# Performance work log

Hardware: AMD Instinct MI355X
Metric: run time of the kernel (lower is better)

The kernel has to match this reference:

```python
import jax, jax.numpy as jnp
import numpy as np

K = 5            # top-k prototypes
EMBED = 256      # per-pixel embedding dim
HIDDEN = 512     # MLP hidden dim
N_LIB = 16384    # lab index size
N_BANDS = 224    # spectral bands of prototype spectra


def setup_inputs() -> dict:
    key = jax.random.key(0)
    ks = jax.random.split(key, 12)
    b, h, w = 2, 128, 128
    inp = {
        "features": jax.random.normal(ks[0], (b, h, w, EMBED), dtype=jnp.float32),
        # score_proj MLP: embed -> hidden -> k
        "w1_s": jax.random.normal(ks[1], (EMBED, HIDDEN), dtype=jnp.float32) / np.sqrt(EMBED),
        "b1_s": jnp.zeros((HIDDEN,), dtype=jnp.float32),
        "w2_s": jax.random.normal(ks[2], (HIDDEN, K), dtype=jnp.float32) / np.sqrt(HIDDEN),
        "b2_s": jnp.zeros((K,), dtype=jnp.float32),
        # abundance_proj MLP: embed+k -> hidden -> k+2
        "w1_a": jax.random.normal(ks[3], (EMBED + K, HIDDEN), dtype=jnp.float32) / np.sqrt(EMBED + K),
        "b1_a": jnp.zeros((HIDDEN,), dtype=jnp.float32),
        "w2_a": jax.random.normal(ks[4], (HIDDEN, K + 2), dtype=jnp.float32) / np.sqrt(HIDDEN),
        "b2_a": jnp.zeros((K + 2,), dtype=jnp.float32),
        # LabIndex library embeddings (cosine-similarity index) and prototype spectra
        "lab_library": jax.random.normal(ks[5], (N_LIB, EMBED), dtype=jnp.float32),
        "prototype_spectra": jax.random.normal(ks[6], (N_LIB, N_BANDS), dtype=jnp.float32),
    }
    return inp


def _mlp(x, w1, b1, w2, b2):
    return jnp.maximum(x @ w1 + b1, 0.0) @ w2 + b2


def reference(features, w1_s, b1_s, w2_s, b2_s, w1_a, b1_a, w2_a, b2_a,
              lab_library, prototype_spectra):
    b, h, w, c = features.shape
    flat = features.reshape(-1, c)                      # [P, C]

    scores = _mlp(flat, w1_s, b1_s, w2_s, b2_s)         # [P, K]

    # batched kNN query (replaces per-pixel Python loop); cosine similarity top-k
    eps = 1e-12
    fn = flat / (jnp.linalg.norm(flat, axis=-1, keepdims=True) + eps)
    ln = lab_library / (jnp.linalg.norm(lab_library, axis=-1, keepdims=True) + eps)
    sims = fn @ ln.T                                    # [P, N_LIB]
    cand_sims, cand_ids = jax.lax.top_k(sims, K)        # [P, K] each

    fused = jnp.concatenate([flat, scores], axis=-1)    # [P, C+K]
    abundance_logits = _mlp(fused, w1_a, b1_a, w2_a, b2_a)  # [P, K+2]
    abundances = jax.nn.softmax(abundance_logits, axis=-1)

    protos = prototype_spectra[cand_ids]                # [P, K, N_BANDS]
    recon = jnp.sum(abundances[:, :K, None] * protos, axis=1)  # [P, N_BANDS]

    best = jnp.argmax(abundances[:, :K], axis=-1)       # [P]
    dominant = jnp.take_along_axis(cand_ids, best[:, None], axis=1)[:, 0]

    return (dominant.reshape(b, h, w),
            abundances.reshape(b, h, w, -1),
            recon.reshape(b, h, w, -1),
            cand_sims.reshape(b, h, w, -1))
```

## Files before the change

kernel.cpp:

```cpp
#include <hip/hip_runtime.h>
#include <math.h>

#define EMB 256
#define HID 512
#define KTOP 5
#define NLIB 16384
#define NB 224
#define P_TOT 32768

#define OUT_DOM ((size_t)0)
#define OUT_AB  ((size_t)P_TOT)
#define OUT_RE  ((size_t)8 * P_TOT)
#define OUT_CS  ((size_t)232 * P_TOT)

#define WS_SCORES 0
#define WS_INVL   (P_TOT * KTOP * 4)
#define WS_IDS8   (WS_INVL + NLIB * 4)
#define WS_CIDS   (WS_IDS8 + P_TOT * 8 * 4)
#define WS_LAB    (WS_CIDS + P_TOT * 5 * 4)

typedef __attribute__((ext_vector_type(8))) short short8;
typedef __attribute__((ext_vector_type(4))) float f32x4;
typedef __attribute__((ext_vector_type(16))) float f32x16;

__device__ __forceinline__ unsigned short f2bf(float x) {
  unsigned int u = __float_as_uint(x);
  u += 0x7fffu + ((u >> 16) & 1u);
  return (unsigned short)(u >> 16);
}
__device__ __forceinline__ float bf2f(unsigned short b) {
  return __uint_as_float(((unsigned int)b) << 16);
}

__device__ __forceinline__ bool better_(float v, int vi, float e, int ei) {
  return (v > e) || ((v == e) && (vi < ei));
}
__device__ __forceinline__ bool betterd_(double v, int vi, double e, int ei) {
  return (v > e) || ((v == e) && (vi < ei));
}

__device__ __forceinline__ void ins5_(float& s0, int& d0, float& s1, int& d1,
                                      float& s2, int& d2, float& s3, int& d3,
                                      float& s4, int& d4, float v, int vi) {
  if (!better_(v, vi, s4, d4)) return;
  s4 = v; d4 = vi;
  if (better_(s4, d4, s3, d3)) {
    float tf = s3; int td = d3; s3 = s4; d3 = d4; s4 = tf; d4 = td;
    if (better_(s3, d3, s2, d2)) {
      tf = s2; td = d2; s2 = s3; d2 = d3; s3 = tf; d3 = td;
      if (better_(s2, d2, s1, d1)) {
        tf = s1; td = d1; s1 = s2; d1 = d2; s2 = tf; d2 = td;
        if (better_(s1, d1, s0, d0)) {
          tf = s0; td = d0; s0 = s1; d0 = d1; s1 = tf; d1 = td;
        }
      }
    }
  }
}

__device__ __forceinline__ void ins8_(float m[8], int n[8], float v, int vi) {
  if (!better_(v, vi, m[7], n[7])) return;
  m[7] = v; n[7] = vi;
  #pragma unroll
  for (int q = 7; q >= 1; --q) {
    if (better_(m[q], n[q], m[q - 1], n[q - 1])) {
      float tf = m[q - 1]; m[q - 1] = m[q]; m[q] = tf;
      int td = n[q - 1]; n[q - 1] = n[q]; n[q] = td;
    }
  }
}

__global__ __launch_bounds__(64) void labsplit_kernel(const float* __restrict__ lab,
                                                      char* __restrict__ wslab) {
  const int row = blockIdx.x;
  const int lane = threadIdx.x;
  const int k16 = lane >> 2, sub = lane & 3;
  float4 v = *(const float4*)(lab + (size_t)row * EMB + k16 * 16 + sub * 4);
  ushort4 ph, pl;
  ph.x = f2bf(v.x); pl.x = f2bf(v.x - bf2f(ph.x));
  ph.y = f2bf(v.y); pl.y = f2bf(v.y - bf2f(ph.y));
  ph.z = f2bf(v.z); pl.z = f2bf(v.z - bf2f(ph.z));
  ph.w = f2bf(v.w); pl.w = f2bf(v.w - bf2f(ph.w));
  const size_t cbase = (size_t)((row >> 8) * 16 + k16) * 16384;
  const size_t off = cbase + (size_t)(row & 255) * 32 + sub * 8;
  *(ushort4*)(wslab + off) = ph;
  *(ushort4*)(wslab + off + 8192) = pl;
}

__global__ __launch_bounds__(64) void libnorm_kernel(const float* __restrict__ lab,
                                                     float* __restrict__ invl) {
  const int row = blockIdx.x;
  const int lane = threadIdx.x;
  float4 v = *(const float4*)(lab + (size_t)row * EMB + lane * 4);
  float s = v.x * v.x + v.y * v.y + v.z * v.z + v.w * v.w;
  #pragma unroll
  for (int off = 32; off >= 1; off >>= 1) s += __shfl_down(s, off);
  if (lane == 0) invl[row] = 1.0f / (sqrtf(s) + 1e-12f);
}

__global__ __launch_bounds__(256) void score_mlp_kernel(
    const float* __restrict__ feat, const float* __restrict__ w1,
    const float* __restrict__ b1, const float* __restrict__ w2,
    const float* __restrict__ b2, float* __restrict__ scores) {
  __shared__ __align__(16) float xs[16 * 264];
  __shared__ __align__(16) float hs[16 * 516];
  const int t = threadIdx.x;
  const int pb = blockIdx.x * 16;

  #pragma unroll
  for (int i = 0; i < 4; ++i) {
    int F = i * 256 + t;
    int p = F >> 6, q = (F & 63) * 4;
    *(float4*)&xs[p * 264 + q] = *(const float4*)(feat + (size_t)(pb + p) * EMB + q);
  }
  __syncthreads();

  const int h0 = t, h1 = t + 256;
  float a0[16], a1[16];
  #pragma unroll
  for (int p = 0; p < 16; ++p) { a0[p] = 0.f; a1[p] = 0.f; }

  for (int i4 = 0; i4 < 64; ++i4) {
    const int i = i4 * 4;
    float w00 = w1[(i + 0) * HID + h0], w01 = w1[(i + 1) * HID + h0];
    float w02 = w1[(i + 2) * HID + h0], w03 = w1[(i + 3) * HID + h0];
    float w10 = w1[(i + 0) * HID + h1], w11 = w1[(i + 1) * HID + h1];
    float w12 = w1[(i + 2) * HID + h1], w13 = w1[(i + 3) * HID + h1];
    #pragma unroll
    for (int p = 0; p < 16; ++p) {
      float4 x = *(const float4*)&xs[p * 264 + i];
      a0[p] = fmaf(x.x, w00, a0[p]); a0[p] = fmaf(x.y, w01, a0[p]);
      a0[p] = fmaf(x.z, w02, a0[p]); a0[p] = fmaf(x.w, w03, a0[p]);
      a1[p] = fmaf(x.x, w10, a1[p]); a1[p] = fmaf(x.y, w11, a1[p]);
      a1[p] = fmaf(x.z, w12, a1[p]); a1[p] = fmaf(x.w, w13, a1[p]);
    }
  }
  const float bb0 = b1[h0], bb1 = b1[h1];
  #pragma unroll
  for (int p = 0; p < 16; ++p) {
    hs[p * 516 + h0] = fmaxf(a0[p] + bb0, 0.f);
    hs[p * 516 + h1] = fmaxf(a1[p] + bb1, 0.f);
  }
  __syncthreads();

  if (t < 80) {
    const int p = t / 5, o = t % 5;
    float acc = b2[o];
    for (int h4 = 0; h4 < 128; ++h4) {
      float4 hv = *(const float4*)&hs[p * 516 + h4 * 4];
      acc = fmaf(hv.x, w2[(h4 * 4 + 0) * 5 + o], acc);
      acc = fmaf(hv.y, w2[(h4 * 4 + 1) * 5 + o], acc);
      acc = fmaf(hv.z, w2[(h4 * 4 + 2) * 5 + o], acc);
      acc = fmaf(hv.w, w2[(h4 * 4 + 3) * 5 + o], acc);
    }
    scores[(size_t)(pb + p) * 5 + o] = acc;
  }
}

__global__ __launch_bounds__(512, 1) void sims_topk_kernel(
    const float* __restrict__ feat, const char* __restrict__ wslab,
    const float* __restrict__ invl, int* __restrict__ ids8) {
  extern __shared__ char smem[];
  char* fhi = smem;
  char* flo = smem + 65536;
  char* lb0 = smem + 131072;
  char* lb1 = smem + 147456;
  const int t = threadIdx.x;
  const int l = t & 63, w = t >> 6;
  const int q = w & 3, h = w >> 2;
  const int pb = blockIdx.x * 128;

  {
    const int px = t >> 2, q4 = t & 3;
    const int pxs = px & 31;
    const float* src = feat + (size_t)(pb + px) * EMB + q4 * 64;
    #pragma unroll
    for (int j = 0; j < 8; ++j) {
      const int slot = q4 * 8 + j;
      float4 v0 = *(const float4*)(src + j * 8);
      float4 v1 = *(const float4*)(src + j * 8 + 4);
      float vv[8] = {v0.x, v0.y, v0.z, v0.w, v1.x, v1.y, v1.z, v1.w};
      unsigned int ph[4], pl[4];
      #pragma unroll
      for (int e = 0; e < 4; ++e) {
        unsigned short ha = f2bf(vv[2 * e]), hb = f2bf(vv[2 * e + 1]);
        unsigned short la = f2bf(vv[2 * e] - bf2f(ha));
        unsigned short lb = f2bf(vv[2 * e + 1] - bf2f(hb));
        ph[e] = (unsigned int)ha | ((unsigned int)hb << 16);
        pl[e] = (unsigned int)la | ((unsigned int)lb << 16);
      }
      const int off = px * 512 + (slot ^ pxs) * 16;
      *(uint4*)(fhi + off) = make_uint4(ph[0], ph[1], ph[2], ph[3]);
      *(uint4*)(flo + off) = make_uint4(pl[0], pl[1], pl[2], pl[3]);
    }
  }

  #pragma unroll
  for (int j = 0; j < 2; ++j) {
    const int off = (j * 8 + w) * 1024;
    __builtin_amdgcn_global_load_lds(
        (const __attribute__((address_space(1))) unsigned int*)(wslab + off + l * 16),
        (__attribute__((address_space(3))) unsigned int*)(lb0 + off), 16, 0, 0);
  }

  f32x16 acc[2][2];
  #pragma unroll
  for (int mi = 0; mi < 2; ++mi)
    #pragma unroll
    for (int nj = 0; nj < 2; ++nj)
      #pragma unroll
      for (int r = 0; r < 16; ++r) acc[mi][nj][r] = 0.f;

  float ts[2][5]; int ti[2][5];
  #pragma unroll
  for (int nj = 0; nj < 2; ++nj)
    #pragma unroll
    for (int e = 0; e < 5; ++e) { ts[nj][e] = -3.0e38f; ti[nj][e] = 0x7fffffff; }

  __syncthreads();

  for (int it = 0; it < 1024; ++it) {
    const char* cur = (it & 1) ? lb1 : lb0;
    char* nxt = (it & 1) ? lb0 : lb1;

    if (it + 1 < 1024) {
      const char* g = wslab + (size_t)(it + 1) * 16384;
      #pragma unroll
      for (int j = 0; j < 2; ++j) {
        const int off = (j * 8 + w) * 1024;
        __builtin_amdgcn_global_load_lds(
            (const __attribute__((address_space(1))) unsigned int*)(g + off + l * 16),
            (__attribute__((address_space(3))) unsigned int*)(nxt + off), 16, 0, 0);
      }
    }

    short8 ah[2], al[2];
    #pragma unroll
    for (int mi = 0; mi < 2; ++mi) {
      const int off = (q * 64 + mi * 32 + (l & 31)) * 32 + (l >> 5) * 16;
      ah[mi] = *(const short8*)(cur + off);
      al[mi] = *(const short8*)(cur + 8192 + off);
    }
    const int k16 = it & 15;
    #pragma unroll
    for (int nj = 0; nj < 2; ++nj) {
      const int px = h * 64 + nj * 32 + (l & 31);
      const int boff = px * 512 + (((k16 * 2 + (l >> 5)) ^ (px & 31)) * 16);
      const short8 bh = *(const short8*)(fhi + boff);
      const short8 bl = *(const short8*)(flo + boff);
      #pragma unroll
      for (int mi = 0; mi < 2; ++mi) {
        acc[mi][nj] = __builtin_amdgcn_mfma_f32_32x32x16_bf16(ah[mi], bh, acc[mi][nj], 0, 0, 0);
        acc[mi][nj] = __builtin_amdgcn_mfma_f32_32x32x16_bf16(ah[mi], bl, acc[mi][nj], 0, 0, 0);
        acc[mi][nj] = __builtin_amdgcn_mfma_f32_32x32x16_bf16(al[mi], bh, acc[mi][nj], 0, 0, 0);
      }
    }

    if (k16 == 15) {
      const int gbase = (it >> 4) * 256 + q * 64;
      #pragma unroll
      for (int mi = 0; mi < 2; ++mi) {
        #pragma unroll
        for (int g4 = 0; g4 < 4; ++g4) {
          const int rbase = gbase + mi * 32 + g4 * 8 + (l >> 5) * 4;
          const f32x4 il = *(const f32x4*)(invl + rbase);
          #pragma unroll
          for (int nj = 0; nj < 2; ++nj) {
            #pragma unroll
            for (int rr = 0; rr < 4; ++rr) {
              const float v = acc[mi][nj][g4 * 4 + rr] * il[rr];
              ins5_(ts[nj][0], ti[nj][0], ts[nj][1], ti[nj][1], ts[nj][2], ti[nj][2],
                    ts[nj][3], ti[nj][3], ts[nj][4], ti[nj][4], v, rbase + rr);
            }
          }
        }
      }
      #pragma unroll
      for (int mi = 0; mi < 2; ++mi)
        #pragma unroll
        for (int nj = 0; nj < 2; ++nj)
          #pragma unroll
          for (int r = 0; r < 16; ++r) acc[mi][nj][r] = 0.f;
    }
    __syncthreads();
  }

  float* simsL = (float*)smem;
  int* idsL = (int*)(smem + 128 * 41 * 4);
  #pragma unroll
  for (int nj = 0; nj < 2; ++nj) {
    const int px = h * 64 + nj * 32 + (l & 31);
    const int col = (q * 2 + (l >> 5)) * 5;
    #pragma unroll
    for (int e = 0; e < 5; ++e) {
      simsL[px * 41 + col + e] = ts[nj][e];
      idsL[px * 41 + col + e] = ti[nj][e];
    }
  }
  __syncthreads();

  if (t < 128) {
    float m[8]; int n[8];
    #pragma unroll
    for (int j = 0; j < 8; ++j) { m[j] = -3.0e38f; n[j] = 0x7fffffff; }
    for (int c = 0; c < 40; ++c)
      ins8_(m, n, simsL[t * 41 + c], idsL[t * 41 + c]);
    const int gp = pb + t;
    #pragma unroll
    for (int j = 0; j < 8; ++j) ids8[(size_t)gp * 8 + j] = n[j];
  }
}

__global__ __launch_bounds__(256) void refine_kernel(
    const float* __restrict__ feat, const float* __restrict__ lab,
    const int* __restrict__ ids8, float* __restrict__ out,
    int* __restrict__ cids) {
  const int t = threadIdx.x;
  const int lane = t & 63;
  const int p = blockIdx.x * 4 + (t >> 6);

  float4 f = *(const float4*)(feat + (size_t)p * EMB + lane * 4);
  const double fx = f.x, fy = f.y, fz = f.z, fw = f.w;
  double sf = fx * fx + fy * fy + fz * fz + fw * fw;

  int id[8];
  #pragma unroll
  for (int j = 0; j < 8; ++j) id[j] = ids8[(size_t)p * 8 + j];

  double dot[8], sl[8];
  #pragma unroll
  for (int j = 0; j < 8; ++j) {
    float4 lv = *(const float4*)(lab + (size_t)id[j] * EMB + lane * 4);
    const double lx = lv.x, ly = lv.y, lz = lv.z, lw = lv.w;
    dot[j] = fma(fx, lx, fma(fy, ly, fma(fz, lz, fw * lw)));
    sl[j]  = fma(lx, lx, fma(ly, ly, fma(lz, lz, lw * lw)));
  }
  #pragma unroll
  for (int off = 32; off >= 1; off >>= 1) {
    sf += __shfl_xor(sf, off);
    #pragma unroll
    for (int j = 0; j < 8; ++j) {
      dot[j] += __shfl_xor(dot[j], off);
      sl[j]  += __shfl_xor(sl[j], off);
    }
  }
  if (lane == 0) {
    const double invf = 1.0 / (sqrt(sf) + 1e-12);
    double s[8];
    #pragma unroll
    for (int j = 0; j < 8; ++j)
      s[j] = dot[j] * (1.0 / (sqrt(sl[j]) + 1e-12)) * invf;
    #pragma unroll
    for (int pass = 0; pass < 7; ++pass) {
      #pragma unroll
      for (int i = 0; i < 7; ++i) {
        if (i < 7 - pass) {
          if (betterd_(s[i + 1], id[i + 1], s[i], id[i])) {
            double tv = s[i]; s[i] = s[i + 1]; s[i + 1] = tv;
            int td = id[i]; id[i] = id[i + 1]; id[i + 1] = td;
          }
        }
      }
    }
    #pragma unroll
    for (int k = 0; k < 5; ++k) {
      out[OUT_CS + (size_t)p * 5 + k] = (float)s[k];
      cids[(size_t)p * 5 + k] = id[k];
    }
  }
}

__global__ __launch_bounds__(256) void abund_kernel(
    const float* __restrict__ feat, const float* __restrict__ scores,
    const float* __restrict__ w1, const float* __restrict__ b1,
    const float* __restrict__ w2, const float* __restrict__ b2,
    const float* __restrict__ proto, const int* __restrict__ cids,
    float* __restrict__ out) {
  __shared__ __align__(16) float xs[16 * 264];
  __shared__ __align__(16) float hs[16 * 520];
  __shared__ float scs[16 * 5];
  __shared__ float lo[16 * 8];
  __shared__ float sAB[16 * 8];
  __shared__ int ids_s[16 * 5];
  const int t = threadIdx.x;
  const int pb = blockIdx.x * 16;

  #pragma unroll
  for (int i = 0; i < 4; ++i) {
    int F = i * 256 + t;
    int p = F >> 6, q = (F & 63) * 4;
    *(float4*)&xs[p * 264 + q] = *(const float4*)(feat + (size_t)(pb + p) * EMB + q);
  }
  if (t < 80) scs[t] = scores[(size_t)(pb + t / 5) * 5 + (t % 5)];
  __syncthreads();

  const int h0 = t, h1 = t + 256;
  float a0[16], a1[16];
  #pragma unroll
  for (int p = 0; p < 16; ++p) { a0[p] = 0.f; a1[p] = 0.f; }

  for (int i4 = 0; i4 < 64; ++i4) {
    const int i = i4 * 4;
    float w00 = w1[(i + 0) * HID + h0], w01 = w1[(i + 1) * HID + h0];
    float w02 = w1[(i + 2) * HID + h0], w03 = w1[(i + 3) * HID + h0];
    float w10 = w1[(i + 0) * HID + h1], w11 = w1[(i + 1) * HID + h1];
    float w12 = w1[(i + 2) * HID + h1], w13 = w1[(i + 3) * HID + h1];
    #pragma unroll
    for (int p = 0; p < 16; ++p) {
      float4 x = *(const float4*)&xs[p * 264 + i];
      a0[p] = fmaf(x.x, w00, a0[p]); a0[p] = fmaf(x.y, w01, a0[p]);
      a0[p] = fmaf(x.z, w02, a0[p]); a0[p] = fmaf(x.w, w03, a0[p]);
      a1[p] = fmaf(x.x, w10, a1[p]); a1[p] = fmaf(x.y, w11, a1[p]);
      a1[p] = fmaf(x.z, w12, a1[p]); a1[p] = fmaf(x.w, w13, a1[p]);
    }
  }
  #pragma unroll
  for (int r = 0; r < 5; ++r) {
    float wA = w1[(256 + r) * HID + h0], wB = w1[(256 + r) * HID + h1];
    #pragma unroll
    for (int p = 0; p < 16; ++p) {
      float x = scs[p * 5 + r];
      a0[p] = fmaf(x, wA, a0[p]);
      a1[p] = fmaf(x, wB, a1[p]);
    }
  }
  const float bb0 = b1[h0], bb1 = b1[h1];
  #pragma unroll
  for (int p = 0; p < 16; ++p) {
    hs[p * 520 + h0] = fmaxf(a0[p] + bb0, 0.f);
    hs[p * 520 + h1] = fmaxf(a1[p] + bb1, 0.f);
  }
  __syncthreads();

  if (t < 112) {
    const int p = t / 7, o = t % 7;
    float acc = b2[o];
    for (int h4 = 0; h4 < 128; ++h4) {
      float4 hv = *(const float4*)&hs[p * 520 + h4 * 4];
      acc = fmaf(hv.x, w2[(h4 * 4 + 0) * 7 + o], acc);
      acc = fmaf(hv.y, w2[(h4 * 4 + 1) * 7 + o], acc);
      acc = fmaf(hv.z, w2[(h4 * 4 + 2) * 7 + o], acc);
      acc = fmaf(hv.w, w2[(h4 * 4 + 3) * 7 + o], acc);
    }
    lo[p * 8 + o] = acc;
  }
  __syncthreads();

  if (t < 16) {
    const int p = t, gp = pb + t;
    float m = lo[p * 8 + 0];
    #pragma unroll
    for (int o = 1; o < 7; ++o) m = fmaxf(m, lo[p * 8 + o]);
    float e[7]; float ssum = 0.f;
    #pragma unroll
    for (int o = 0; o < 7; ++o) { e[o] = expf(lo[p * 8 + o] - m); ssum += e[o]; }
    const float inv = 1.0f / ssum;
    #pragma unroll
    for (int o = 0; o < 7; ++o) {
      float a = e[o] * inv;
      sAB[p * 8 + o] = a;
      out[OUT_AB + (size_t)gp * 7 + o] = a;
    }
    int best = 0; float bv = lo[p * 8 + 0];
    #pragma unroll
    for (int k = 1; k < 5; ++k)
      if (lo[p * 8 + k] > bv) { bv = lo[p * 8 + k]; best = k; }
    #pragma unroll
    for (int k = 0; k < 5; ++k) ids_s[p * 5 + k] = cids[(size_t)gp * 5 + k];
    out[OUT_DOM + gp] = (float)ids_s[p * 5 + best];
  }
  __syncthreads();

  {
    const int p = t >> 4, l16 = t & 15;
    const int gp = pb + p, bz = l16 * 14;
    float r[14];
    #pragma unroll
    for (int j = 0; j < 14; ++j) r[j] = 0.f;
    #pragma unroll
    for (int k = 0; k < 5; ++k) {
      const int idk = ids_s[p * 5 + k];
      const float a = sAB[p * 8 + k];
      const float* pr = proto + (size_t)idk * NB + bz;
      #pragma unroll
      for (int j = 0; j < 14; ++j) r[j] = fmaf(a, pr[j], r[j]);
    }
    #pragma unroll
    for (int j = 0; j < 14; ++j) out[OUT_RE + (size_t)gp * NB + bz + j] = r[j];
  }
}

extern "C" void kernel_launch(void* const* d_in, const int* in_sizes, int n_in,
                              void* d_out, int out_size, void* d_ws, size_t ws_size,
                              hipStream_t stream) {
  (void)in_sizes; (void)n_in; (void)out_size; (void)ws_size;
  const float* feat  = (const float*)d_in[0];
  const float* w1_s  = (const float*)d_in[1];
  const float* b1_s  = (const float*)d_in[2];
  const float* w2_s  = (const float*)d_in[3];
  const float* b2_s  = (const float*)d_in[4];
  const float* w1_a  = (const float*)d_in[5];
  const float* b1_a  = (const float*)d_in[6];
  const float* w2_a  = (const float*)d_in[7];
  const float* b2_a  = (const float*)d_in[8];
  const float* lab   = (const float*)d_in[9];
  const float* proto = (const float*)d_in[10];
  float* out = (float*)d_out;
  char* ws = (char*)d_ws;
  float* wscores = (float*)(ws + WS_SCORES);
  float* winvl   = (float*)(ws + WS_INVL);
  int*   wids8   = (int*)(ws + WS_IDS8);
  int*   wcids   = (int*)(ws + WS_CIDS);
  char*  wlab    = ws + WS_LAB;

  (void)hipFuncSetAttribute(reinterpret_cast<const void*>(sims_topk_kernel),
                            hipFuncAttributeMaxDynamicSharedMemorySize, 163840);

  labsplit_kernel<<<dim3(NLIB), dim3(64), 0, stream>>>(lab, wlab);
  libnorm_kernel<<<dim3(NLIB), dim3(64), 0, stream>>>(lab, winvl);
  score_mlp_kernel<<<dim3(P_TOT / 16), dim3(256), 0, stream>>>(
      feat, w1_s, b1_s, w2_s, b2_s, wscores);
  sims_topk_kernel<<<dim3(P_TOT / 128), dim3(512), 163840, stream>>>(
      feat, wlab, winvl, wids8);
  refine_kernel<<<dim3(P_TOT / 4), dim3(256), 0, stream>>>(
      feat, lab, wids8, out, wcids);
  abund_kernel<<<dim3(P_TOT / 16), dim3(256), 0, stream>>>(
      feat, wscores, w1_a, b1_a, w2_a, b2_a, proto, wcids, out);
}
```

Measured before the change: 1.531 ms.

## Load library MFMA fragments directly to registers, dropping LDS staging and per-step barriers

The library split layout is changed so that each lane can load its bf16 hi/lo A-fragments straight from global memory into registers. A two-stage register double buffer replaces the LDS double buffer and the __syncthreads on every k-step. The MFMA issue order is also interleaved across independent accumulators, and the feature staging loads are reordered for better coalescing. This removes LDS traffic, barrier stalls and 32KB of shared memory, at the cost of relying on L2/cache to serve the repeated global A loads and holding more live registers.

```diff
diff --git a/kernel.cpp b/kernel.cpp
--- a/kernel.cpp
+++ b/kernel.cpp
@@ -18,6 +18,7 @@
 #define WS_IDS8   (WS_INVL + NLIB * 4)
 #define WS_CIDS   (WS_IDS8 + P_TOT * 8 * 4)
 #define WS_LAB    (WS_CIDS + P_TOT * 5 * 4)
+#define LABLO_OFF ((size_t)NLIB * 32 * 16)
 
 typedef __attribute__((ext_vector_type(8))) short short8;
 typedef __attribute__((ext_vector_type(4))) float f32x4;
@@ -74,17 +75,18 @@
                                                       char* __restrict__ wslab) {
   const int row = blockIdx.x;
   const int lane = threadIdx.x;
-  const int k16 = lane >> 2, sub = lane & 3;
-  float4 v = *(const float4*)(lab + (size_t)row * EMB + k16 * 16 + sub * 4);
+  float4 v = *(const float4*)(lab + (size_t)row * EMB + lane * 4);
   ushort4 ph, pl;
   ph.x = f2bf(v.x); pl.x = f2bf(v.x - bf2f(ph.x));
   ph.y = f2bf(v.y); pl.y = f2bf(v.y - bf2f(ph.y));
   ph.z = f2bf(v.z); pl.z = f2bf(v.z - bf2f(ph.z));
   ph.w = f2bf(v.w); pl.w = f2bf(v.w - bf2f(ph.w));
-  const size_t cbase = (size_t)((row >> 8) * 16 + k16) * 16384;
-  const size_t off = cbase + (size_t)(row & 255) * 32 + sub * 8;
+  const int k16 = lane >> 2;
+  const int khalf = (lane >> 1) & 1;
+  const int b8 = (lane & 1) * 8;
+  const size_t off = (size_t)k16 * (NLIB * 32) + (size_t)row * 32 + khalf * 16 + b8;
   *(ushort4*)(wslab + off) = ph;
-  *(ushort4*)(wslab + off + 8192) = pl;
+  *(ushort4*)(wslab + LABLO_OFF + off) = pl;
 }
 
 __global__ __launch_bounds__(64) void libnorm_kernel(const float* __restrict__ lab,
@@ -163,8 +165,6 @@
   extern __shared__ char smem[];
   char* fhi = smem;
   char* flo = smem + 65536;
-  char* lb0 = smem + 131072;
-  char* lb1 = smem + 147456;
   const int t = threadIdx.x;
   const int l = t & 63, w = t >> 6;
   const int q = w & 3, h = w >> 2;
@@ -173,12 +173,12 @@
   {
     const int px = t >> 2, q4 = t & 3;
     const int pxs = px & 31;
-    const float* src = feat + (size_t)(pb + px) * EMB + q4 * 64;
+    const float* src = feat + (size_t)(pb + px) * EMB;
     #pragma unroll
     for (int j = 0; j < 8; ++j) {
-      const int slot = q4 * 8 + j;
-      float4 v0 = *(const float4*)(src + j * 8);
-      float4 v1 = *(const float4*)(src + j * 8 + 4);
+      const int slot = j * 4 + q4;
+      float4 v0 = *(const float4*)(src + slot * 8);
+      float4 v1 = *(const float4*)(src + slot * 8 + 4);
       float vv[8] = {v0.x, v0.y, v0.z, v0.w, v1.x, v1.y, v1.z, v1.w};
       unsigned int ph[4], pl[4];
       #pragma unroll
@@ -195,14 +195,6 @@
     }
   }
 
-  #pragma unroll
-  for (int j = 0; j < 2; ++j) {
-    const int off = (j * 8 + w) * 1024;
-    __builtin_amdgcn_global_load_lds(
-        (const __attribute__((address_space(1))) unsigned int*)(wslab + off + l * 16),
-        (__attribute__((address_space(3))) unsigned int*)(lb0 + off), 16, 0, 0);
-  }
-
   f32x16 acc[2][2];
   #pragma unroll
   for (int mi = 0; mi < 2; ++mi)
@@ -217,80 +209,93 @@
     #pragma unroll
     for (int e = 0; e < 5; ++e) { ts[nj][e] = -3.0e38f; ti[nj][e] = 0x7fffffff; }
 
-  __syncthreads();
-
-  for (int it = 0; it < 1024; ++it) {
-    const char* cur = (it & 1) ? lb1 : lb0;
-    char* nxt = (it & 1) ? lb0 : lb1;
-
-    if (it + 1 < 1024) {
-      const char* g = wslab + (size_t)(it + 1) * 16384;
-      #pragma unroll
-      for (int j = 0; j < 2; ++j) {
-        const int off = (j * 8 + w) * 1024;
-        __builtin_amdgcn_global_load_lds(
-            (const __attribute__((address_space(1))) unsigned int*)(g + off + l * 16),
-            (__attribute__((address_space(3))) unsigned int*)(nxt + off), 16, 0, 0);
-      }
-    }
-
-    short8 ah[2], al[2];
-    #pragma unroll
-    for (int mi = 0; mi < 2; ++mi) {
-      const int off = (q * 64 + mi * 32 + (l & 31)) * 32 + (l >> 5) * 16;
-      ah[mi] = *(const short8*)(cur + off);
-      al[mi] = *(const short8*)(cur + 8192 + off);
-    }
-    const int k16 = it & 15;
-    #pragma unroll
-    for (int nj = 0; nj < 2; ++nj) {
-      const int px = h * 64 + nj * 32 + (l & 31);
-      const int boff = px * 512 + (((k16 * 2 + (l >> 5)) ^ (px & 31)) * 16);
-      const short8 bh = *(const short8*)(fhi + boff);
-      const short8 bl = *(const short8*)(flo + boff);
-      #pragma unroll
-      for (int mi = 0; mi < 2; ++mi) {
-        acc[mi][nj] = __builtin_amdgcn_mfma_f32_32x32x16_bf16(ah[mi], bh, acc[mi][nj], 0, 0, 0);
-        acc[mi][nj] = __builtin_amdgcn_mfma_f32_32x32x16_bf16(ah[mi], bl, acc[mi][nj], 0, 0, 0);
-        acc[mi][nj] = __builtin_amdgcn_mfma_f32_32x32x16_bf16(al[mi], bh, acc[mi][nj], 0, 0, 0);
-      }
-    }
-
-    if (k16 == 15) {
-      const int gbase = (it >> 4) * 256 + q * 64;
-      #pragma unroll
-      for (int mi = 0; mi < 2; ++mi) {
-        #pragma unroll
-        for (int g4 = 0; g4 < 4; ++g4) {
-          const int rbase = gbase + mi * 32 + g4 * 8 + (l >> 5) * 4;
-          const f32x4 il = *(const f32x4*)(invl + rbase);
-          #pragma unroll
-          for (int nj = 0; nj < 2; ++nj) {
-            #pragma unroll
-            for (int rr = 0; rr < 4; ++rr) {
-              const float v = acc[mi][nj][g4 * 4 + rr] * il[rr];
-              ins5_(ts[nj][0], ti[nj][0], ts[nj][1], ti[nj][1], ts[nj][2], ti[nj][2],
-                    ts[nj][3], ti[nj][3], ts[nj][4], ti[nj][4], v, rbase + rr);
-            }
-          }
-        }
-      }
-      #pragma unroll
-      for (int mi = 0; mi < 2; ++mi)
-        #pragma unroll
-        for (int nj = 0; nj < 2; ++nj)
-          #pragma unroll
-          for (int r = 0; r < 16; ++r) acc[mi][nj][r] = 0.f;
-    }
-    __syncthreads();
-  }
-
+  const size_t laneoff = (size_t)(q * 64 + (l & 31)) * 32 + (l >> 5) * 16;
+  const int lk = l >> 5;
+  const int pxs = l & 31;
+  const int pxb0 = (h * 64 + (l & 31)) * 512;
+  const int pxb1 = (h * 64 + 32 + (l & 31)) * 512;
+
+#define LOADA(H0, H1, L0, L1, IT) do {                                        \
+    const int k16_ = (IT) & 15, st_ = (IT) >> 4;                              \
+    const char* pa_ = wslab + (size_t)k16_ * (NLIB * 32) + (size_t)st_ * 8192 \
+                      + laneoff;                                              \
+    H0 = *(const short8*)(pa_);                                               \
+    H1 = *(const short8*)(pa_ + 1024);                                        \
+    L0 = *(const short8*)(pa_ + LABLO_OFF);                                   \
+    L1 = *(const short8*)(pa_ + LABLO_OFF + 1024);                            \
+  } while (0)
+
+#define BODY(IT, H0, H1, L0, L1) do {                                         \
+    const int k16_ = (IT) & 15;                                               \
+    const int bswz_ = (((k16_ * 2 + lk) ^ pxs) * 16);                         \
+    const short8 bh0 = *(const short8*)(fhi + pxb0 + bswz_);                  \
+    const short8 bl0 = *(const short8*)(flo + pxb0 + bswz_);                  \
+    const short8 bh1 = *(const short8*)(fhi + pxb1 + bswz_);                  \
+    const short8 bl1 = *(const short8*)(flo + pxb1 + bswz_);                  \
+    acc[0][0] = __builtin_amdgcn_mfma_f32_32x32x16_bf16(H0, bh0, acc[0][0], 0, 0, 0); \
+    acc[0][1] = __builtin_amdgcn_mfma_f32_32x32x16_bf16(H0, bh1, acc[0][1], 0, 0, 0); \
+    acc[1][0] = __builtin_amdgcn_mfma_f32_32x32x16_bf16(H1, bh0, acc[1][0], 0, 0, 0); \
+    acc[1][1] = __builtin_amdgcn_mfma_f32_32x32x16_bf16(H1, bh1, acc[1][1], 0, 0, 0); \
+    acc[0][0] = __builtin_amdgcn_mfma_f32_32x32x16_bf16(H0, bl0, acc[0][0], 0, 0, 0); \
+    acc[0][1] = __builtin_amdgcn_mfma_f32_32x32x16_bf16(H0, bl1, acc[0][1], 0, 0, 0); \
+    acc[1][0] = __builtin_amdgcn_mfma_f32_32x32x16_bf16(L1, bh0, acc[1][0], 0, 0, 0); \
+    acc[1][1] = __builtin_amdgcn_mfma_f32_32x32x16_bf16(L1, bh1, acc[1][1], 0, 0, 0); \
+    acc[0][0] = __builtin_amdgcn_mfma_f32_32x32x16_bf16(L0, bh0, acc[0][0], 0, 0, 0); \
+    acc[0][1] = __builtin_amdgcn_mfma_f32_32x32x16_bf16(L0, bh1, acc[0][1], 0, 0, 0); \
+    acc[1][0] = __builtin_amdgcn_mfma_f32_32x32x16_bf16(H1, bl0, acc[1][0], 0, 0, 0); \
+    acc[1][1] = __builtin_amdgcn_mfma_f32_32x32x16_bf16(H1, bl1, acc[1][1], 0, 0, 0); \
+    if (k16_ == 15) {                                                         \
+      const int gbase_ = ((IT) >> 4) * 256 + q * 64;                          \
+      _Pragma("unroll")                                                       \
+      for (int mi = 0; mi < 2; ++mi) {                                        \
+        _Pragma("unroll")                                                     \
+        for (int g4 = 0; g4 < 4; ++g4) {                                      \
+          const int rbase_ = gbase_ + mi * 32 + g4 * 8 + lk * 4;              \
+          const f32x4 il_ = *(const f32x4*)(invl + rbase_);                   \
+          _Pragma("unroll")                                                   \
+          for (int nj = 0; nj < 2; ++nj) {                                    \
+            _Pragma("unroll")                                                 \
+            for (int rr = 0; rr < 4; ++rr) {                                  \
+              const float v_ = acc[mi][nj][g4 * 4 + rr] * il_[rr];            \
+              ins5_(ts[nj][0], ti[nj][0], ts[nj][1], ti[nj][1], ts[nj][2],    \
+                    ti[nj][2], ts[nj][3], ti[nj][3], ts[nj][4], ti[nj][4],    \
+                    v_, rbase_ + rr);                                         \
+            }                                                                 \
+          }                                                                   \
+        }                                                                     \
+      }                                                                       \
+      _Pragma("unroll")                                                       \
+      for (int mi = 0; mi < 2; ++mi)                                          \
+        _Pragma("unroll")                                                     \
+        for (int nj = 0; nj < 2; ++nj)                                        \
+          _Pragma("unroll")                                                   \
+          for (int r = 0; r < 16; ++r) acc[mi][nj][r] = 0.f;                  \
+    }                                                                         \
+  } while (0)
+
+  short8 a0h0, a0h1, a0l0, a0l1;
+  short8 a1h0, a1h1, a1l0, a1l1;
+  LOADA(a0h0, a0h1, a0l0, a0l1, 0);
+
+  __syncthreads();
+
+  #pragma unroll 1
+  for (int it2 = 0; it2 < 1024; it2 += 2) {
+    LOADA(a1h0, a1h1, a1l0, a1l1, it2 + 1);
+    BODY(it2, a0h0, a0h1, a0l0, a0l1);
+    if (it2 + 2 < 1024) LOADA(a0h0, a0h1, a0l0, a0l1, it2 + 2);
+    BODY(it2 + 1, a1h0, a1h1, a1l0, a1l1);
+  }
+#undef LOADA
+#undef BODY
+
+  __syncthreads();
   float* simsL = (float*)smem;
   int* idsL = (int*)(smem + 128 * 41 * 4);
   #pragma unroll
   for (int nj = 0; nj < 2; ++nj) {
     const int px = h * 64 + nj * 32 + (l & 31);
-    const int col = (q * 2 + (l >> 5)) * 5;
+    const int col = (q * 2 + lk) * 5;
     #pragma unroll
     for (int e = 0; e < 5; ++e) {
       simsL[px * 41 + col + e] = ts[nj][e];
@@ -514,13 +519,13 @@
   char*  wlab    = ws + WS_LAB;
 
   (void)hipFuncSetAttribute(reinterpret_cast<const void*>(sims_topk_kernel),
-                            hipFuncAttributeMaxDynamicSharedMemorySize, 163840);
+                            hipFuncAttributeMaxDynamicSharedMemorySize, 131072);
 
   labsplit_kernel<<<dim3(NLIB), dim3(64), 0, stream>>>(lab, wlab);
   libnorm_kernel<<<dim3(NLIB), dim3(64), 0, stream>>>(lab, winvl);
   score_mlp_kernel<<<dim3(P_TOT / 16), dim3(256), 0, stream>>>(
       feat, w1_s, b1_s, w2_s, b2_s, wscores);
-  sims_topk_kernel<<<dim3(P_TOT / 128), dim3(512), 163840, stream>>>(
+  sims_topk_kernel<<<dim3(P_TOT / 128), dim3(512), 131072, stream>>>(
       feat, wlab, winvl, wids8);
   refine_kernel<<<dim3(P_TOT / 4), dim3(256), 0, stream>>>(
       feat, lab, wids8, out, wcids);
```

New measurement: 1.359 ms. -11.2%, faster.
